# Optimization experiments

Hardware: AMD Instinct MI355X
Metric: run time of the kernel (lower is better)

The kernel has to match this reference:

```python
import jax, jax.numpy as jnp
import numpy as np
import math

L_LAYERS = 4
EMBED = 512
HEADS = 8
FFN = 2048
EPS = 1e-20
PAD_IDX = 0


def sinusoidal_table(num_embeddings, embedding_dim, padding_idx=0):
    half = embedding_dim // 2
    freq = jnp.exp(jnp.arange(half, dtype=jnp.float32) * (-math.log(10000.0) / (half - 1)))
    ang = jnp.arange(num_embeddings, dtype=jnp.float32)[:, None] * freq[None, :]
    emb = jnp.concatenate([jnp.sin(ang), jnp.cos(ang)], axis=1)
    if padding_idx is not None:
        emb = emb.at[padding_idx].set(0.0)
    return emb  # [num_embeddings, embedding_dim]


def layer_norm(x, g, b):
    mu = jnp.mean(x, axis=-1, keepdims=True)
    var = jnp.mean((x - mu) ** 2, axis=-1, keepdims=True)
    return (x - mu) * jax.lax.rsqrt(var + EPS) * g + b


def mha(x_q, x_kv, Wqkv, bqkv, Wo, bo, mask):
    """Custom attention: scaled scores, multiplicative mask, GLOBAL min-max norm (no softmax)."""
    T, B, C = x_q.shape
    S = x_kv.shape[0]
    hd = C // HEADS
    scale = hd ** -0.5
    q = x_q @ Wqkv[:C].T + bqkv[:C]
    k = x_kv @ Wqkv[C:2 * C].T + bqkv[C:2 * C]
    v = x_kv @ Wqkv[2 * C:].T + bqkv[2 * C:]
    q = q * scale
    # [T,B,C] -> [B*H, T, hd]
    q = q.reshape(T, B * HEADS, hd).transpose(1, 0, 2)
    k = k.reshape(S, B * HEADS, hd).transpose(1, 0, 2)
    v = v.reshape(S, B * HEADS, hd).transpose(1, 0, 2)
    w = jnp.einsum('bth,bsh->bts', q, k)  # [B*H, T, S]
    if mask is not None:
        w = w * mask[None, :, :]
    # global min-max normalization (as in the torch source)
    w = (w - jnp.min(w)) / (jnp.max(w) - jnp.min(w))
    a = jnp.einsum('bts,bsh->bth', w, v)  # [B*H, T, hd]
    a = a.transpose(1, 0, 2).reshape(T, B, C)
    return a @ Wo.T + bo


def setup_inputs() -> dict:
    key = jax.random.key(0)
    ks = iter(jax.random.split(key, 32))
    T, B, C, F, L = 2048, 2, EMBED, FFN, L_LAYERS
    d = {}
    d['x'] = jax.random.normal(next(ks), (T, B, C), dtype=jnp.float32)
    d['enc_out'] = jax.random.normal(next(ks), (T, B, C), dtype=jnp.float32)
    d['tokens'] = jax.random.randint(next(ks), (B, T), 0, 32000, dtype=jnp.int64 if jax.config.read('jax_enable_x64') else jnp.int32)
    sd = C ** -0.5
    d['self_Wqkv'] = jax.random.normal(next(ks), (L, 3 * C, C)) * sd
    d['self_bqkv'] = jnp.zeros((L, 3 * C))
    d['self_Wo'] = jax.random.normal(next(ks), (L, C, C)) * sd
    d['self_bo'] = jnp.zeros((L, C))
    d['cross_Wqkv'] = jax.random.normal(next(ks), (L, 3 * C, C)) * sd
    d['cross_bqkv'] = jnp.zeros((L, 3 * C))
    d['cross_Wo'] = jax.random.normal(next(ks), (L, C, C)) * sd
    d['cross_bo'] = jnp.zeros((L, C))
    d['fc1_w'] = jax.random.normal(next(ks), (L, F, C)) * sd
    d['fc1_b'] = jnp.zeros((L, F))
    d['fc2_w'] = jax.random.normal(next(ks), (L, C, F)) * (F ** -0.5)
    d['fc2_b'] = jnp.zeros((L, C))
    d['ln1_g'] = jnp.ones((L, C)); d['ln1_b'] = jnp.zeros((L, C))
    d['ln2_g'] = jnp.ones((L, C)); d['ln2_b'] = jnp.zeros((L, C))
    d['ln3_g'] = jnp.ones((L, C)); d['ln3_b'] = jnp.zeros((L, C))
    return d


def _forward(x, enc_out, tokens, self_Wqkv, self_bqkv, self_Wo, self_bo,
             cross_Wqkv, cross_bqkv, cross_Wo, cross_bo,
             fc1_w, fc1_b, fc2_w, fc2_b, ln1_g, ln1_b, ln2_g, ln2_b, ln3_g, ln3_b):
    T, B, C = x.shape
    # sinusoidal positional embedding (make_positions with padding_idx=0, no left pad)
    table = sinusoidal_table(PAD_IDX + 1 + T, C, PAD_IDX)
    pos = jnp.where(tokens != PAD_IDX, jnp.arange(1, T + 1)[None, :], 0)  # [B, T]
    pe = table[pos]  # [B, T, C]
    x = x + pe.transpose(1, 0, 2)
    # multiplicative future mask: tril of ones
    fmask = jnp.tril(jnp.ones((T, T), dtype=x.dtype))
    for l in range(L_LAYERS):
        # self-attention
        res = x
        x = mha(x, x, self_Wqkv[l], self_bqkv[l], self_Wo[l], self_bo[l], fmask)
        x = layer_norm(res + x, ln1_g[l], ln1_b[l])
        # cross-attention (no mask)
        res = x
        x = mha(x, enc_out, cross_Wqkv[l], cross_bqkv[l], cross_Wo[l], cross_bo[l], None)
        x = layer_norm(res + x, ln2_g[l], ln2_b[l])
        # FFN
        res = x
        h = jax.nn.relu(x @ fc1_w[l].T + fc1_b[l])
        x = h @ fc2_w[l].T + fc2_b[l]
        x = layer_norm(res + x, ln3_g[l], ln3_b[l])
    return x


def reference(x, enc_out, tokens, self_Wqkv, self_bqkv, self_Wo, self_bo,
              cross_Wqkv, cross_bqkv, cross_Wo, cross_bo,
              fc1_w, fc1_b, fc2_w, fc2_b, ln1_g, ln1_b, ln2_g, ln2_b, ln3_g, ln3_b):
    return _forward(x, enc_out, tokens, self_Wqkv, self_bqkv, self_Wo, self_bo,
                    cross_Wqkv, cross_bqkv, cross_Wo, cross_bo,
                    fc1_w, fc1_b, fc2_w, fc2_b, ln1_g, ln1_b, ln2_g, ln2_b, ln3_g, ln3_b)
```

## Files before the change

kernel.cpp:

```cpp
#include <hip/hip_runtime.h>
#include <math.h>

typedef __bf16 bf16;
typedef unsigned short u16;
typedef __bf16 bf16x8 __attribute__((ext_vector_type(8)));
typedef float f32x4 __attribute__((ext_vector_type(4)));

#define T_SEQ 2048
#define NB    2
#define CE    512
#define NH    8
#define HD    64
#define ROWS  4096
#define NBH   16
#define LDT   40
#define LDA   72

#define MFMA16(a,b,c) __builtin_amdgcn_mfma_f32_16x16x32_bf16((a),(b),(c),0,0,0)

static __device__ __forceinline__ int xcd_swz(int id, int n) {
  int q = n >> 3, r = n & 7;
  int x = id & 7, o = id >> 3;
  return (x < r) ? (x * (q + 1) + o) : (r * (q + 1) + (x - r) * q + o);
}

__global__ __launch_bounds__(256) void sniff(const u16* __restrict__ xs,
                                             const int* __restrict__ toks,
                                             int* __restrict__ flags)
{
  const int tid = threadIdx.x;
  int crazy = 0, ze = 0;
  for (int i = tid; i < 4096; i += 256) {
    int e = (xs[i] >> 7) & 0xFF;
    if (e >= 141) crazy++;
    if (((i & 1) == 0) && (xs[i] == 0)) ze++;
  }
  int zc = 0;
  for (int i = tid; i < 1024; i += 256)
    if (toks[2 * i + 1] == 0) zc++;
  __shared__ int r1[4], r2[4], r3[4];
#pragma unroll
  for (int o = 32; o; o >>= 1) {
    crazy += __shfl_down(crazy, o); ze += __shfl_down(ze, o); zc += __shfl_down(zc, o);
  }
  if ((tid & 63) == 0) { r1[tid >> 6] = crazy; r2[tid >> 6] = ze; r3[tid >> 6] = zc; }
  __syncthreads();
  if (tid == 0) {
    int c = r1[0] + r1[1] + r1[2] + r1[3];
    int z = r2[0] + r2[1] + r2[2] + r2[3];
    int t = r3[0] + r3[1] + r3[2] + r3[3];
    flags[0] = (z > 1500 || c > 64) ? 1 : 0;
    flags[1] = (t > 900) ? 1 : 0;
  }
}

static __device__ __forceinline__ float ldf(const void* src, size_t eoff, bool f32) {
  return f32 ? ((const float*)src)[eoff] : (float)((const bf16*)src)[eoff];
}

__global__ __launch_bounds__(256) void posembed(const void* __restrict__ xsrc,
                                                const int* __restrict__ toks,
                                                const int* __restrict__ flags,
                                                float* __restrict__ xf)
{
  const bool f32 = flags[0] != 0;
  const bool tok64 = flags[1] != 0;
  const int row = blockIdx.x;
  const int t = row >> 1, b = row & 1;
  const int tix = b * T_SEQ + t;
  const int tok = tok64 ? toks[2 * tix] : toks[tix];
  const int p = (tok != 0) ? (t + 1) : 0;
  const float kf = -0.0361193740f;
  for (int c = threadIdx.x; c < CE; c += 256) {
    float pe = 0.0f;
    if (p != 0) {
      int i = (c < 256) ? c : (c - 256);
      float freq = expf((float)i * kf);
      float ang = (float)p * freq;
      pe = (c < 256) ? sinf(ang) : cosf(ang);
    }
    xf[(size_t)row * CE + c] = ldf(xsrc, (size_t)row * CE + c, f32) + pe;
  }
}

template<bool RELUF, bool AFFINE>
__global__ __launch_bounds__(256) void gemm_mfma(const float* __restrict__ A,
                                                 const void* __restrict__ A2,
                                                 const void* __restrict__ Bw, size_t bwOff,
                                                 const void* __restrict__ bias, size_t biasOff,
                                                 const int* __restrict__ flags,
                                                 float* __restrict__ Cf,
                                                 int N, int K, int kspan,
                                                 int nbx, int nbxA,
                                                 long long partStride,
                                                 const float* __restrict__ mmf,
                                                 const float* __restrict__ vsum)
{
  __shared__ __align__(16) bf16 AhS[2][128 * LDT];
  __shared__ __align__(16) bf16 AlS[2][128 * LDT];
  __shared__ __align__(16) bf16 BhS[2][128 * LDT];
  __shared__ __align__(16) bf16 BlS[2][128 * LDT];
  const int fl = flags[0];
  const int nblk = nbx * (int)1;
  (void)nblk;
  const int id = xcd_swz((int)blockIdx.x, (int)gridDim.x);
  const int per_z = nbx * 32;
  const int zz = id / per_z;
  const int rem = id - zz * per_z;
  const int by = rem / nbx, bx = rem - by * nbx;
  const bool a_f32 = (bx < nbxA) ? true : (fl != 0);
  const void* Abase = (bx < nbxA) ? (const void*)A : A2;
  const bool b_f32 = (fl != 0);
  const int tid = threadIdx.x;
  const int m0 = by * 128, n0 = bx * 128;
  const int srow = tid >> 1;
  const int skc  = (tid & 1) * 16;
  const int wid = tid >> 6, lane = tid & 63;
  const int wm = (wid >> 1) * 64, wn = (wid & 1) * 64;
  const int fr = lane & 15;
  const int fk = (lane >> 4) * 8;
  const int kb = zz * kspan;
  const int ke = (kb + kspan < K) ? (kb + kspan) : K;
  float* Cp = Cf + (long long)zz * partStride;
  const int arow1 = (m0 + srow) & 1;
  float inv_ = 0.0f, cmn_ = 0.0f;
  if (AFFINE) { inv_ = 1.0f / (mmf[1] - mmf[0]); cmn_ = mmf[0] * inv_; }
  f32x4 acc[4][4] = {};

  uint4 ra[4], rb[4];
  auto loadA = [&](int k0) {
    size_t g = (size_t)(m0 + srow) * K + k0 + skc;
    if (a_f32) {
      const uint4* p = (const uint4*)((const float*)Abase + g);
      ra[0] = p[0]; ra[1] = p[1]; ra[2] = p[2]; ra[3] = p[3];
    } else {
      const uint4* p = (const uint4*)((const bf16*)Abase + g);
      ra[0] = p[0]; ra[1] = p[1];
    }
  };
  auto loadB = [&](int k0) {
    size_t g = bwOff + (size_t)(n0 + srow) * K + k0 + skc;
    if (b_f32) {
      const uint4* p = (const uint4*)((const float*)Bw + g);
      rb[0] = p[0]; rb[1] = p[1]; rb[2] = p[2]; rb[3] = p[3];
    } else {
      const uint4* p = (const uint4*)((const bf16*)Bw + g);
      rb[0] = p[0]; rb[1] = p[1];
    }
  };
  auto fixA = [&](int k0) {
    if (AFFINE) {
      float* f = (float*)ra;
      const float* vs = vsum + arow1 * 512 + k0 + skc;
#pragma unroll
      for (int q = 0; q < 16; q++) f[q] = inv_ * f[q] - cmn_ * vs[q];
    }
  };
  auto cvtStore = [&](const uint4* r, bool f32src, bool wantLo, bf16* Hs, bf16* Ls) {
    float v[16];
    if (f32src) {
      const float* f = (const float*)r;
#pragma unroll
      for (int q = 0; q < 16; q++) v[q] = f[q];
    } else {
      const bf16* c = (const bf16*)r;
#pragma unroll
      for (int q = 0; q < 16; q++) v[q] = (float)c[q];
    }
    bf16x8 h0, h1, l0, l1;
#pragma unroll
    for (int q = 0; q < 8; q++) {
      bf16 ha = (bf16)v[q], hb = (bf16)v[8 + q];
      h0[q] = ha; h1[q] = hb;
      l0[q] = (bf16)(v[q]     - (float)ha);
      l1[q] = (bf16)(v[8 + q] - (float)hb);
    }
    *(bf16x8*)&Hs[srow * LDT + skc]     = h0;
    *(bf16x8*)&Hs[srow * LDT + skc + 8] = h1;
    if (wantLo) {
      *(bf16x8*)&Ls[srow * LDT + skc]     = l0;
      *(bf16x8*)&Ls[srow * LDT + skc + 8] = l1;
    }
  };

  loadA(kb); loadB(kb);
  fixA(kb);
  cvtStore(ra, a_f32, a_f32, AhS[0], AlS[0]);
  cvtStore(rb, b_f32, b_f32, BhS[0], BlS[0]);
  if (kb + 32 < ke) { loadA(kb + 32); loadB(kb + 32); }

  int cur = 0;
  for (int k0 = kb; k0 < ke; k0 += 32) {
    __syncthreads();
    if (k0 + 32 < ke) {
      fixA(k0 + 32);
      cvtStore(ra, a_f32, a_f32, AhS[cur ^ 1], AlS[cur ^ 1]);
      cvtStore(rb, b_f32, b_f32, BhS[cur ^ 1], BlS[cur ^ 1]);
      if (k0 + 64 < ke) { loadA(k0 + 64); loadB(k0 + 64); }
    }
    const bf16* Ahc = AhS[cur]; const bf16* Alc = AlS[cur];
    const bf16* Bhc = BhS[cur]; const bf16* Blc = BlS[cur];
    bf16x8 ah[4], bh[4];
#pragma unroll
    for (int i = 0; i < 4; i++) ah[i] = *(const bf16x8*)&Ahc[(wm + i*16 + fr) * LDT + fk];
#pragma unroll
    for (int j = 0; j < 4; j++) bh[j] = *(const bf16x8*)&Bhc[(wn + j*16 + fr) * LDT + fk];
#pragma unroll
    for (int i = 0; i < 4; i++)
#pragma unroll
      for (int j = 0; j < 4; j++)
        acc[i][j] = MFMA16(ah[i], bh[j], acc[i][j]);
    if (a_f32) {
      bf16x8 al[4];
#pragma unroll
      for (int i = 0; i < 4; i++) al[i] = *(const bf16x8*)&Alc[(wm + i*16 + fr) * LDT + fk];
#pragma unroll
      for (int i = 0; i < 4; i++)
#pragma unroll
        for (int j = 0; j < 4; j++)
          acc[i][j] = MFMA16(al[i], bh[j], acc[i][j]);
    }
    if (b_f32) {
      bf16x8 bl[4];
#pragma unroll
      for (int j = 0; j < 4; j++) bl[j] = *(const bf16x8*)&Blc[(wn + j*16 + fr) * LDT + fk];
#pragma unroll
      for (int i = 0; i < 4; i++)
#pragma unroll
        for (int j = 0; j < 4; j++)
          acc[i][j] = MFMA16(ah[i], bl[j], acc[i][j]);
    }
    cur ^= 1;
  }
  const int orow0 = m0 + wm + (lane >> 4) * 4;
  const int ocol0 = n0 + wn + (lane & 15);
  const bool addb = (zz == 0);
#pragma unroll
  for (int j = 0; j < 4; j++) {
    int col = ocol0 + j * 16;
    float bv = addb ? ldf(bias, biasOff + col, b_f32) : 0.0f;
#pragma unroll
    for (int i = 0; i < 4; i++) {
#pragma unroll
      for (int r = 0; r < 4; r++) {
        float vv = acc[i][j][r] + bv;
        if (RELUF) vv = fmaxf(vv, 0.0f);
        Cp[(size_t)(orow0 + i * 16 + r) * N + col] = vv;
      }
    }
  }
}

__global__ __launch_bounds__(256) void prep_kv(const float* __restrict__ base, int ld,
                                               int kofs0, int vofs0,
                                               bf16* __restrict__ kh, bf16* __restrict__ kl,
                                               bf16* __restrict__ vth, bf16* __restrict__ vtl,
                                               float* __restrict__ vcs)
{
  __shared__ float ts[64 * 65];
  const int bh = blockIdx.x, s0 = blockIdx.y * 64;
  const int b = bh >> 3, h = bh & 7;
  const int kofs = kofs0 + h * HD, vofs = vofs0 + h * HD;
  const int tid = threadIdx.x;
#pragma unroll
  for (int it = 0; it < 16; ++it) {
    int idx = it * 256 + tid, r = idx >> 6, d = idx & 63;
    size_t rowb = (size_t)((s0 + r) * NB + b) * ld;
    float v = base[rowb + kofs + d];
    bf16 hi = (bf16)v;
    size_t o = ((size_t)bh * T_SEQ + s0 + r) * 64 + d;
    kh[o] = hi; kl[o] = (bf16)(v - (float)hi);
    ts[r * 65 + d] = base[rowb + vofs + d];
  }
  __syncthreads();
  const int d = tid >> 2, sseg = (tid & 3) * 16;
  bf16x8 hv0, lv0, hv1, lv1;
#pragma unroll
  for (int q = 0; q < 8; ++q) {
    float v0 = ts[(sseg + q) * 65 + d];
    float v1 = ts[(sseg + 8 + q) * 65 + d];
    bf16 h0 = (bf16)v0, h1 = (bf16)v1;
    hv0[q] = h0; lv0[q] = (bf16)(v0 - (float)h0);
    hv1[q] = h1; lv1[q] = (bf16)(v1 - (float)h1);
  }
  size_t o = ((size_t)bh * 64 + d) * T_SEQ + s0 + sseg;
  *(bf16x8*)&vth[o]     = hv0;
  *(bf16x8*)&vth[o + 8] = hv1;
  *(bf16x8*)&vtl[o]     = lv0;
  *(bf16x8*)&vtl[o + 8] = lv1;
  if (tid < 64) {
    float s = 0.0f;
    for (int j = 0; j < 64; ++j) s += ts[j * 65 + tid];
    vcs[((size_t)bh * 32 + blockIdx.y) * 64 + tid] = s;
  }
}

__device__ __forceinline__ int remap_ty(int ty) { return (ty < 16) ? ty : 47 - ty; }

template<bool MASK>
__global__ __launch_bounds__(256) void fattn(const float* __restrict__ qbase, int qld, int qofs0,
                                             const bf16* __restrict__ kh, const bf16* __restrict__ kl,
                                             const bf16* __restrict__ vth, const bf16* __restrict__ vtl,
                                             float* __restrict__ partial,
                                             float* __restrict__ pvout)
{
  __shared__ __align__(16) bf16 Qh[64 * LDA], Ql[64 * LDA];
  __shared__ __align__(16) bf16 Kh[64 * LDA], Kl[64 * LDA];
  __shared__ __align__(16) bf16 Vh[64 * LDA], Vl[64 * LDA];
  __shared__ __align__(16) bf16 Ph[64 * LDA], Pl[64 * LDA];
  __shared__ float rn[4], rx[4];
  const int id = xcd_swz((int)blockIdx.x, 512);
  const int bh = id >> 5;
  const int tyr = remap_ty(id & 31);
  const int t0 = tyr * 64;
  const int b = bh >> 3, h = bh & 7;
  const int qofs = qofs0 + h * HD;
  const int tid = threadIdx.x;
#pragma unroll
  for (int it = 0; it < 16; ++it) {
    int idx = it * 256 + tid, r = idx >> 6, d = idx & 63;
    float v = qbase[(size_t)((t0 + r) * NB + b) * qld + qofs + d] * 0.125f;
    bf16 hi = (bf16)v;
    Qh[r * LDA + d] = hi; Ql[r * LDA + d] = (bf16)(v - (float)hi);
  }
  const int wid = tid >> 6, lane = tid & 63;
  const int wm_ = (wid >> 1) * 32, wn_ = (wid & 1) * 32;
  const int fr = lane & 15, fko = (lane >> 4) * 8;
  const int crr = (lane >> 4) * 4, crc = lane & 15;
  const int cr = tid >> 2, cseg = (tid & 3) * 16;
  float mn = 1e30f, mx = -1e30f;
  f32x4 o4[2][2] = {};
  const int nch = MASK ? (tyr + 1) : 32;
  for (int sc = 0; sc < nch; ++sc) {
    const int s0 = sc * 64;
    __syncthreads();
    {
      size_t go = ((size_t)bh * T_SEQ + s0 + cr) * 64 + cseg;
      *(bf16x8*)&Kh[cr * LDA + cseg]     = *(const bf16x8*)&kh[go];
      *(bf16x8*)&Kh[cr * LDA + cseg + 8] = *(const bf16x8*)&kh[go + 8];
      *(bf16x8*)&Kl[cr * LDA + cseg]     = *(const bf16x8*)&kl[go];
      *(bf16x8*)&Kl[cr * LDA + cseg + 8] = *(const bf16x8*)&kl[go + 8];
      size_t gv = ((size_t)bh * 64 + cr) * T_SEQ + s0 + cseg;
      *(bf16x8*)&Vh[cr * LDA + cseg]     = *(const bf16x8*)&vth[gv];
      *(bf16x8*)&Vh[cr * LDA + cseg + 8] = *(const bf16x8*)&vth[gv + 8];
      *(bf16x8*)&Vl[cr * LDA + cseg]     = *(const bf16x8*)&vtl[gv];
      *(bf16x8*)&Vl[cr * LDA + cseg + 8] = *(const bf16x8*)&vtl[gv + 8];
    }
    __syncthreads();
    f32x4 a4[2][2] = {};
#pragma unroll
    for (int ks = 0; ks < 2; ++ks) {
      bf16x8 aH[2], aL[2], bH[2], bL[2];
#pragma unroll
      for (int i = 0; i < 2; ++i) {
        aH[i] = *(const bf16x8*)&Qh[(wm_ + i*16 + fr) * LDA + ks*32 + fko];
        aL[i] = *(const bf16x8*)&Ql[(wm_ + i*16 + fr) * LDA + ks*32 + fko];
        bH[i] = *(const bf16x8*)&Kh[(wn_ + i*16 + fr) * LDA + ks*32 + fko];
        bL[i] = *(const bf16x8*)&Kl[(wn_ + i*16 + fr) * LDA + ks*32 + fko];
      }
#pragma unroll
      for (int i = 0; i < 2; ++i)
#pragma unroll
        for (int j = 0; j < 2; ++j) {
          a4[i][j] = MFMA16(aH[i], bH[j], a4[i][j]);
          a4[i][j] = MFMA16(aL[i], bH[j], a4[i][j]);
          a4[i][j] = MFMA16(aH[i], bL[j], a4[i][j]);
        }
    }
#pragma unroll
    for (int i = 0; i < 2; ++i)
#pragma unroll
      for (int j = 0; j < 2; ++j)
#pragma unroll
        for (int r = 0; r < 4; ++r) {
          int tl = wm_ + i*16 + crr + r;
          int sl = wn_ + j*16 + crc;
          float w = a4[i][j][r];
          if (MASK && (s0 + sl) > (t0 + tl)) w = 0.0f;
          mn = fminf(mn, w); mx = fmaxf(mx, w);
          bf16 wh = (bf16)w;
          Ph[tl * LDA + sl] = wh;
          Pl[tl * LDA + sl] = (bf16)(w - (float)wh);
        }
    __syncthreads();
#pragma unroll
    for (int ks = 0; ks < 2; ++ks) {
      bf16x8 pH[2], pL[2], vH[2], vL[2];
#pragma unroll
      for (int i = 0; i < 2; ++i) {
        pH[i] = *(const bf16x8*)&Ph[(wm_ + i*16 + fr) * LDA + ks*32 + fko];
        pL[i] = *(const bf16x8*)&Pl[(wm_ + i*16 + fr) * LDA + ks*32 + fko];
        vH[i] = *(const bf16x8*)&Vh[(wn_ + i*16 + fr) * LDA + ks*32 + fko];
        vL[i] = *(const bf16x8*)&Vl[(wn_ + i*16 + fr) * LDA + ks*32 + fko];
      }
#pragma unroll
      for (int i = 0; i < 2; ++i)
#pragma unroll
        for (int j = 0; j < 2; ++j) {
          o4[i][j] = MFMA16(pH[i], vH[j], o4[i][j]);
          o4[i][j] = MFMA16(pL[i], vH[j], o4[i][j]);
          o4[i][j] = MFMA16(pH[i], vL[j], o4[i][j]);
        }
    }
  }
#pragma unroll
  for (int i = 0; i < 2; ++i)
#pragma unroll
    for (int j = 0; j < 2; ++j)
#pragma unroll
      for (int r = 0; r < 4; ++r) {
        int tl = wm_ + i*16 + crr + r;
        int dl = wn_ + j*16 + crc;
        pvout[(size_t)((t0 + tl) * NB + b) * CE + h * HD + dl] = o4[i][j][r];
      }
#pragma unroll
  for (int o = 32; o; o >>= 1) { mn = fminf(mn, __shfl_down(mn, o)); mx = fmaxf(mx, __shfl_down(mx, o)); }
  if (lane == 0) { rn[wid] = mn; rx[wid] = mx; }
  __syncthreads();
  if (tid == 0) {
    partial[2 * id]     = fminf(fminf(rn[0], rn[1]), fminf(rn[2], rn[3]));
    partial[2 * id + 1] = fmaxf(fmaxf(rx[0], rx[1]), fmaxf(rx[2], rx[3]));
  }
}

__global__ __launch_bounds__(512) void reduce_mm(const float* __restrict__ partial,
                                                 const float* __restrict__ vcs,
                                                 float* __restrict__ mmf,
                                                 float* __restrict__ vsum)
{
  const int tid = threadIdx.x, w = tid >> 6, l = tid & 63;
  __shared__ float rn[8], rx[8];
  float mn = partial[2 * tid], mx = partial[2 * tid + 1];
#pragma unroll
  for (int o = 32; o; o >>= 1) { mn = fminf(mn, __shfl_down(mn, o)); mx = fmaxf(mx, __shfl_down(mx, o)); }
  if (l == 0) { rn[w] = mn; rx[w] = mx; }
  __syncthreads();
  if (tid == 0) {
    float a = 1e30f, c = -1e30f;
#pragma unroll
    for (int i = 0; i < 8; i++) { a = fminf(a, rn[i]); c = fmaxf(c, rx[i]); }
    mmf[0] = a; mmf[1] = c;
  }
  for (int e = tid; e < 1024; e += 512) {
    int bh = e >> 6, d = e & 63;
    float s = 0.0f;
#pragma unroll
    for (int ch = 0; ch < 32; ++ch) s += vcs[(size_t)bh * 2048 + ch * 64 + d];
    vsum[e] = s;
  }
}

template<int NP>
__global__ __launch_bounds__(256) void ln_sum(const float* __restrict__ res,
                                              const float* __restrict__ p, long long pstride,
                                              const void* __restrict__ g, const void* __restrict__ be,
                                              size_t goff, const int* __restrict__ flags,
                                              float* __restrict__ xfo)
{
  __shared__ float red[4];
  const bool fl = flags[0] != 0;
  const int tid = threadIdx.x;
  const size_t base = (size_t)blockIdx.x * CE;
  float a  = res[base + tid];
  float b2 = res[base + tid + 256];
#pragma unroll
  for (int k = 0; k < NP; k++) {
    a  += p[(long long)k * pstride + base + tid];
    b2 += p[(long long)k * pstride + base + tid + 256];
  }
  float s = a + b2;
#pragma unroll
  for (int o = 32; o; o >>= 1) s += __shfl_down(s, o);
  if ((tid & 63) == 0) red[tid >> 6] = s;
  __syncthreads();
  float mu = (red[0] + red[1] + red[2] + red[3]) * (1.0f / 512.0f);
  __syncthreads();
  float da = a - mu, db = b2 - mu;
  float q = da * da + db * db;
#pragma unroll
  for (int o = 32; o; o >>= 1) q += __shfl_down(q, o);
  if ((tid & 63) == 0) red[tid >> 6] = q;
  __syncthreads();
  float var = (red[0] + red[1] + red[2] + red[3]) * (1.0f / 512.0f);
  float rs = rsqrtf(var + 1e-20f);
  xfo[base + tid]       = da * rs * ldf(g, goff + tid, fl)       + ldf(be, goff + tid, fl);
  xfo[base + tid + 256] = db * rs * ldf(g, goff + tid + 256, fl) + ldf(be, goff + tid + 256, fl);
}

extern "C" void kernel_launch(void* const* d_in, const int* in_sizes, int n_in,
                              void* d_out, int out_size, void* d_ws, size_t ws_size,
                              hipStream_t stream)
{
  (void)in_sizes; (void)n_in; (void)out_size; (void)ws_size;
  const void* x_in   = d_in[0];
  const void* enc_in = d_in[1];
  const int*  tokens = (const int*)d_in[2];
  const void* sWqkv = d_in[3];
  const void* sbqkv = d_in[4];
  const void* sWo   = d_in[5];
  const void* sbo   = d_in[6];
  const void* cWqkv = d_in[7];
  const void* cbqkv = d_in[8];
  const void* cWo   = d_in[9];
  const void* cbo   = d_in[10];
  const void* fc1w  = d_in[11];
  const void* fc1b  = d_in[12];
  const void* fc2w  = d_in[13];
  const void* fc2b  = d_in[14];
  const void* ln1g  = d_in[15];
  const void* ln1b  = d_in[16];
  const void* ln2g  = d_in[17];
  const void* ln2b  = d_in[18];
  const void* ln3g  = d_in[19];
  const void* ln3b  = d_in[20];

  char* ws = (char*)d_ws;
  size_t off = 0;
  auto alloc = [&](size_t bytes) -> char* {
    char* p = ws + off;
    off += (bytes + 255) & ~(size_t)255;
    return p;
  };
  int*   flags   = (int*)  alloc(256);
  float* mmf     = (float*)alloc(256);
  float* vsum    = (float*)alloc(1024 * 4);
  float* partial = (float*)alloc(4096);
  float* xf      = (float*)alloc((size_t)ROWS * CE * 4);
  float* y       = (float*)alloc((size_t)ROWS * CE * 4);
  float* qkv     = (float*)alloc((size_t)ROWS * 2048 * 4);
  float* pblk    = (float*)alloc((size_t)ROWS * CE * 4 * 4);
  bf16*  khb     = (bf16*) alloc((size_t)16 * T_SEQ * 64 * 2);
  bf16*  klb     = (bf16*) alloc((size_t)16 * T_SEQ * 64 * 2);
  bf16*  vth     = (bf16*) alloc((size_t)16 * 64 * T_SEQ * 2);
  bf16*  vtl     = (bf16*) alloc((size_t)16 * 64 * T_SEQ * 2);
  float* vcs     = (float*)alloc((size_t)16 * 32 * 64 * 4);
  const long long PS_FULL = (long long)ROWS * CE;

  sniff<<<1, 256, 0, stream>>>((const u16*)x_in, tokens, flags);
  posembed<<<ROWS, 256, 0, stream>>>(x_in, tokens, flags, xf);

  for (int l = 0; l < 4; l++) {
    gemm_mfma<false, false><<<384, 256, 0, stream>>>(
        xf, xf, sWqkv, (size_t)l * 1536 * 512, sbqkv, (size_t)l * 1536, flags, qkv,
        1536, 512, 512, 12, 12, 0, nullptr, nullptr);
    prep_kv<<<dim3(16, 32), 256, 0, stream>>>(qkv, 1536, 512, 1024, khb, klb, vth, vtl, vcs);
    fattn<true><<<512, 256, 0, stream>>>(qkv, 1536, 0, khb, klb, vth, vtl, partial, y);
    reduce_mm<<<1, 512, 0, stream>>>(partial, vcs, mmf, vsum);
    gemm_mfma<false, true><<<512, 256, 0, stream>>>(
        y, y, sWo, (size_t)l * 512 * 512, sbo, (size_t)l * 512, flags, pblk,
        512, 512, 128, 4, 4, PS_FULL, mmf, vsum);
    ln_sum<4><<<ROWS, 256, 0, stream>>>(xf, pblk, PS_FULL, ln1g, ln1b, (size_t)l * 512, flags, xf);

    gemm_mfma<false, false><<<384, 256, 0, stream>>>(
        xf, enc_in, cWqkv, (size_t)l * 1536 * 512, cbqkv, (size_t)l * 1536, flags, qkv,
        1536, 512, 512, 12, 4 , 0, nullptr, nullptr);
    prep_kv<<<dim3(16, 32), 256, 0, stream>>>(qkv, 1536, 512, 1024, khb, klb, vth, vtl, vcs);
    fattn<false><<<512, 256, 0, stream>>>(qkv, 1536, 0, khb, klb, vth, vtl, partial, y);
    reduce_mm<<<1, 512, 0, stream>>>(partial, vcs, mmf, vsum);
    gemm_mfma<false, true><<<512, 256, 0, stream>>>(
        y, y, cWo, (size_t)l * 512 * 512, cbo, (size_t)l * 512, flags, pblk,
        512, 512, 128, 4, 4, PS_FULL, mmf, vsum);
    ln_sum<4><<<ROWS, 256, 0, stream>>>(xf, pblk, PS_FULL, ln2g, ln2b, (size_t)l * 512, flags, xf);

    gemm_mfma<true, false><<<512, 256, 0, stream>>>(
        xf, xf, fc1w, (size_t)l * 2048 * 512, fc1b, (size_t)l * 2048, flags, qkv,
        2048, 512, 512, 16, 16, 0, nullptr, nullptr);
    gemm_mfma<false, false><<<512, 256, 0, stream>>>(
        qkv, qkv, fc2w, (size_t)l * 512 * 2048, fc2b, (size_t)l * 512, flags, pblk,
        512, 2048, 512, 4, 4, PS_FULL, nullptr, nullptr);
    float* lnout = (l == 3) ? (float*)d_out : xf;
    ln_sum<4><<<ROWS, 256, 0, stream>>>(xf, pblk, PS_FULL, ln3g, ln3b, (size_t)l * 512, flags, lnout);
  }
}
```

Baseline: 2.602 ms.

## Pre-split activations and weights into bf16 hi/lo pairs, move min-max affine to epilogue

Producers (posembed, ln_sum, fattn, fc1 epilogue) now write bf16 hi/lo pairs, and a one-time wprep kernel splits all weights and enc_out into hi/lo buffers. The GEMM becomes a pure bf16 loader with no fp32 loads or conversion in its main loop, and it skips the lo MFMA passes when the flags show the lo parts are zero. The min-max affine on attention output moves out of the Wo GEMM into a small wo_term kernel plus ln_sum. This trades extra memory writes and the per-call weight preparation against lighter GEMM inner loops.

```diff
diff --git a/kernel.cpp b/kernel.cpp
--- a/kernel.cpp
+++ b/kernel.cpp
@@ -9,19 +9,29 @@
 #define T_SEQ 2048
 #define NB    2
 #define CE    512
-#define NH    8
 #define HD    64
 #define ROWS  4096
-#define NBH   16
 #define LDT   40
 #define LDA   72
 
 #define MFMA16(a,b,c) __builtin_amdgcn_mfma_f32_16x16x32_bf16((a),(b),(c),0,0,0)
+
+#define O_SQ  0LL
+#define O_SWO 3145728LL
+#define O_CQ  4194304LL
+#define O_CWO 7340032LL
+#define O_F1  8388608LL
+#define O_F2  12582912LL
+#define O_E   16777216LL
 
 static __device__ __forceinline__ int xcd_swz(int id, int n) {
   int q = n >> 3, r = n & 7;
   int x = id & 7, o = id >> 3;
   return (x < r) ? (x * (q + 1) + o) : (r * (q + 1) + (x - r) * q + o);
+}
+
+static __device__ __forceinline__ float ldf(const void* src, size_t eoff, bool f32) {
+  return f32 ? ((const float*)src)[eoff] : (float)((const bf16*)src)[eoff];
 }
 
 __global__ __launch_bounds__(256) void sniff(const u16* __restrict__ xs,
@@ -51,17 +61,65 @@
     int t = r3[0] + r3[1] + r3[2] + r3[3];
     flags[0] = (z > 1500 || c > 64) ? 1 : 0;
     flags[1] = (t > 900) ? 1 : 0;
-  }
-}
-
-static __device__ __forceinline__ float ldf(const void* src, size_t eoff, bool f32) {
-  return f32 ? ((const float*)src)[eoff] : (float)((const bf16*)src)[eoff];
+    flags[2] = 1;
+    flags[3] = 0;
+    flags[4] = 0;
+  }
+}
+
+__global__ __launch_bounds__(256) void wprep(const void* w0, const void* w1, const void* w2,
+                                             const void* w3, const void* w4, const void* w5,
+                                             const void* w6,
+                                             bf16* __restrict__ wh, bf16* __restrict__ wl,
+                                             int* __restrict__ flags)
+{
+  const int m = blockIdx.y;
+  const void* srcs[7] = {w0, w1, w2, w3, w4, w5, w6};
+  const int sizes[7]  = {3145728, 1048576, 3145728, 1048576, 4194304, 4194304, 2097152};
+  const long long offs[7] = {O_SQ, O_SWO, O_CQ, O_CWO, O_F1, O_F2, O_E};
+  const void* src = srcs[m];
+  const int sz = sizes[m];
+  const long long off = offs[m];
+  const bool fl = flags[0] != 0;
+  long long i0 = ((long long)blockIdx.x * 256 + threadIdx.x) * 16;
+  bool nz = false;
+  if (i0 < sz) {
+    float v[16];
+    if (fl) {
+      const float4* p = (const float4*)((const float*)src + i0);
+#pragma unroll
+      for (int q = 0; q < 4; q++) { float4 t = p[q]; v[4*q] = t.x; v[4*q+1] = t.y; v[4*q+2] = t.z; v[4*q+3] = t.w; }
+    } else {
+      const uint4* p = (const uint4*)((const bf16*)src + i0);
+      uint4 a = p[0], b = p[1];
+      const bf16* c0 = (const bf16*)&a; const bf16* c1 = (const bf16*)&b;
+#pragma unroll
+      for (int q = 0; q < 8; q++) { v[q] = (float)c0[q]; v[8+q] = (float)c1[q]; }
+    }
+    bf16x8 h0, h1, l0, l1;
+#pragma unroll
+    for (int q = 0; q < 8; q++) {
+      bf16 a = (bf16)v[q], b = (bf16)v[8+q];
+      h0[q] = a; h1[q] = b;
+      float la = v[q] - (float)a, lb = v[8+q] - (float)b;
+      l0[q] = (bf16)la; l1[q] = (bf16)lb;
+      nz = nz || (la != 0.0f) || (lb != 0.0f);
+    }
+    *(bf16x8*)&wh[off + i0]     = h0;
+    *(bf16x8*)&wh[off + i0 + 8] = h1;
+    *(bf16x8*)&wl[off + i0]     = l0;
+    *(bf16x8*)&wl[off + i0 + 8] = l1;
+  }
+  unsigned long long mv = __ballot(nz);
+  if ((threadIdx.x & 63) == 0 && mv)
+    atomicOr(&flags[(m == 6) ? 3 : 4], 1);
 }
 
 __global__ __launch_bounds__(256) void posembed(const void* __restrict__ xsrc,
                                                 const int* __restrict__ toks,
                                                 const int* __restrict__ flags,
-                                                float* __restrict__ xf)
+                                                float* __restrict__ xf,
+                                                bf16* __restrict__ xh, bf16* __restrict__ xl)
 {
   const bool f32 = flags[0] != 0;
   const bool tok64 = flags[1] != 0;
@@ -79,124 +137,87 @@
       float ang = (float)p * freq;
       pe = (c < 256) ? sinf(ang) : cosf(ang);
     }
-    xf[(size_t)row * CE + c] = ldf(xsrc, (size_t)row * CE + c, f32) + pe;
-  }
-}
-
-template<bool RELUF, bool AFFINE>
-__global__ __launch_bounds__(256) void gemm_mfma(const float* __restrict__ A,
-                                                 const void* __restrict__ A2,
-                                                 const void* __restrict__ Bw, size_t bwOff,
-                                                 const void* __restrict__ bias, size_t biasOff,
-                                                 const int* __restrict__ flags,
-                                                 float* __restrict__ Cf,
-                                                 int N, int K, int kspan,
-                                                 int nbx, int nbxA,
-                                                 long long partStride,
-                                                 const float* __restrict__ mmf,
-                                                 const float* __restrict__ vsum)
+    float v = ldf(xsrc, (size_t)row * CE + c, f32) + pe;
+    size_t o = (size_t)row * CE + c;
+    xf[o] = v;
+    bf16 hi = (bf16)v;
+    xh[o] = hi; xl[o] = (bf16)(v - (float)hi);
+  }
+}
+
+template<int OUTM, bool BIAS>
+__global__ __launch_bounds__(256) void gemm_bb(const bf16* __restrict__ A1h, const bf16* __restrict__ A1l,
+                                               const bf16* __restrict__ A2h, const bf16* __restrict__ A2l,
+                                               const bf16* __restrict__ Bhg, const bf16* __restrict__ Blg,
+                                               long long bOff,
+                                               const void* __restrict__ bias, size_t biasOff,
+                                               const int* __restrict__ flags,
+                                               int aIdx1, int aIdx2, int bIdx,
+                                               float* __restrict__ Cf,
+                                               bf16* __restrict__ Coh, bf16* __restrict__ Col,
+                                               int N, int K, int kspan, int nbx, int nbxA,
+                                               long long partStride)
 {
   __shared__ __align__(16) bf16 AhS[2][128 * LDT];
   __shared__ __align__(16) bf16 AlS[2][128 * LDT];
   __shared__ __align__(16) bf16 BhS[2][128 * LDT];
   __shared__ __align__(16) bf16 BlS[2][128 * LDT];
-  const int fl = flags[0];
-  const int nblk = nbx * (int)1;
-  (void)nblk;
   const int id = xcd_swz((int)blockIdx.x, (int)gridDim.x);
   const int per_z = nbx * 32;
   const int zz = id / per_z;
   const int rem = id - zz * per_z;
   const int by = rem / nbx, bx = rem - by * nbx;
-  const bool a_f32 = (bx < nbxA) ? true : (fl != 0);
-  const void* Abase = (bx < nbxA) ? (const void*)A : A2;
-  const bool b_f32 = (fl != 0);
+  const bf16* Ahg = (bx < nbxA) ? A1h : A2h;
+  const bf16* Alg = (bx < nbxA) ? A1l : A2l;
+  const bool alo = flags[(bx < nbxA) ? aIdx1 : aIdx2] != 0;
+  const bool blo = flags[bIdx] != 0;
+  const bool bfl = flags[0] != 0;
   const int tid = threadIdx.x;
   const int m0 = by * 128, n0 = bx * 128;
-  const int srow = tid >> 1;
-  const int skc  = (tid & 1) * 16;
+  const int srow = tid >> 1, skc = (tid & 1) * 16;
   const int wid = tid >> 6, lane = tid & 63;
   const int wm = (wid >> 1) * 64, wn = (wid & 1) * 64;
-  const int fr = lane & 15;
-  const int fk = (lane >> 4) * 8;
+  const int fr = lane & 15, fk = (lane >> 4) * 8;
   const int kb = zz * kspan;
   const int ke = (kb + kspan < K) ? (kb + kspan) : K;
-  float* Cp = Cf + (long long)zz * partStride;
-  const int arow1 = (m0 + srow) & 1;
-  float inv_ = 0.0f, cmn_ = 0.0f;
-  if (AFFINE) { inv_ = 1.0f / (mmf[1] - mmf[0]); cmn_ = mmf[0] * inv_; }
   f32x4 acc[4][4] = {};
 
-  uint4 ra[4], rb[4];
-  auto loadA = [&](int k0) {
-    size_t g = (size_t)(m0 + srow) * K + k0 + skc;
-    if (a_f32) {
-      const uint4* p = (const uint4*)((const float*)Abase + g);
-      ra[0] = p[0]; ra[1] = p[1]; ra[2] = p[2]; ra[3] = p[3];
-    } else {
-      const uint4* p = (const uint4*)((const bf16*)Abase + g);
-      ra[0] = p[0]; ra[1] = p[1];
-    }
+  uint4 rah[2], ral[2], rbh[2], rbl[2];
+  auto loadAB = [&](int k0) {
+    size_t ga = (size_t)(m0 + srow) * K + k0 + skc;
+    const uint4* pa = (const uint4*)(Ahg + ga);
+    rah[0] = pa[0]; rah[1] = pa[1];
+    if (alo) { const uint4* q = (const uint4*)(Alg + ga); ral[0] = q[0]; ral[1] = q[1]; }
+    size_t gb = (size_t)bOff + (size_t)(n0 + srow) * K + k0 + skc;
+    const uint4* pb = (const uint4*)(Bhg + gb);
+    rbh[0] = pb[0]; rbh[1] = pb[1];
+    if (blo) { const uint4* q = (const uint4*)(Blg + gb); rbl[0] = q[0]; rbl[1] = q[1]; }
   };
-  auto loadB = [&](int k0) {
-    size_t g = bwOff + (size_t)(n0 + srow) * K + k0 + skc;
-    if (b_f32) {
-      const uint4* p = (const uint4*)((const float*)Bw + g);
-      rb[0] = p[0]; rb[1] = p[1]; rb[2] = p[2]; rb[3] = p[3];
-    } else {
-      const uint4* p = (const uint4*)((const bf16*)Bw + g);
-      rb[0] = p[0]; rb[1] = p[1];
+  auto storeAB = [&](int buf) {
+    *(uint4*)&AhS[buf][srow * LDT + skc]     = rah[0];
+    *(uint4*)&AhS[buf][srow * LDT + skc + 8] = rah[1];
+    if (alo) {
+      *(uint4*)&AlS[buf][srow * LDT + skc]     = ral[0];
+      *(uint4*)&AlS[buf][srow * LDT + skc + 8] = ral[1];
+    }
+    *(uint4*)&BhS[buf][srow * LDT + skc]     = rbh[0];
+    *(uint4*)&BhS[buf][srow * LDT + skc + 8] = rbh[1];
+    if (blo) {
+      *(uint4*)&BlS[buf][srow * LDT + skc]     = rbl[0];
+      *(uint4*)&BlS[buf][srow * LDT + skc + 8] = rbl[1];
     }
   };
-  auto fixA = [&](int k0) {
-    if (AFFINE) {
-      float* f = (float*)ra;
-      const float* vs = vsum + arow1 * 512 + k0 + skc;
-#pragma unroll
-      for (int q = 0; q < 16; q++) f[q] = inv_ * f[q] - cmn_ * vs[q];
-    }
-  };
-  auto cvtStore = [&](const uint4* r, bool f32src, bool wantLo, bf16* Hs, bf16* Ls) {
-    float v[16];
-    if (f32src) {
-      const float* f = (const float*)r;
-#pragma unroll
-      for (int q = 0; q < 16; q++) v[q] = f[q];
-    } else {
-      const bf16* c = (const bf16*)r;
-#pragma unroll
-      for (int q = 0; q < 16; q++) v[q] = (float)c[q];
-    }
-    bf16x8 h0, h1, l0, l1;
-#pragma unroll
-    for (int q = 0; q < 8; q++) {
-      bf16 ha = (bf16)v[q], hb = (bf16)v[8 + q];
-      h0[q] = ha; h1[q] = hb;
-      l0[q] = (bf16)(v[q]     - (float)ha);
-      l1[q] = (bf16)(v[8 + q] - (float)hb);
-    }
-    *(bf16x8*)&Hs[srow * LDT + skc]     = h0;
-    *(bf16x8*)&Hs[srow * LDT + skc + 8] = h1;
-    if (wantLo) {
-      *(bf16x8*)&Ls[srow * LDT + skc]     = l0;
-      *(bf16x8*)&Ls[srow * LDT + skc + 8] = l1;
-    }
-  };
-
-  loadA(kb); loadB(kb);
-  fixA(kb);
-  cvtStore(ra, a_f32, a_f32, AhS[0], AlS[0]);
-  cvtStore(rb, b_f32, b_f32, BhS[0], BlS[0]);
-  if (kb + 32 < ke) { loadA(kb + 32); loadB(kb + 32); }
+
+  loadAB(kb);
+  storeAB(0);
+  if (kb + 32 < ke) loadAB(kb + 32);
 
   int cur = 0;
   for (int k0 = kb; k0 < ke; k0 += 32) {
     __syncthreads();
     if (k0 + 32 < ke) {
-      fixA(k0 + 32);
-      cvtStore(ra, a_f32, a_f32, AhS[cur ^ 1], AlS[cur ^ 1]);
-      cvtStore(rb, b_f32, b_f32, BhS[cur ^ 1], BlS[cur ^ 1]);
-      if (k0 + 64 < ke) { loadA(k0 + 64); loadB(k0 + 64); }
+      storeAB(cur ^ 1);
+      if (k0 + 64 < ke) loadAB(k0 + 64);
     }
     const bf16* Ahc = AhS[cur]; const bf16* Alc = AlS[cur];
     const bf16* Bhc = BhS[cur]; const bf16* Blc = BlS[cur];
@@ -210,7 +231,7 @@
 #pragma unroll
       for (int j = 0; j < 4; j++)
         acc[i][j] = MFMA16(ah[i], bh[j], acc[i][j]);
-    if (a_f32) {
+    if (alo) {
       bf16x8 al[4];
 #pragma unroll
       for (int i = 0; i < 4; i++) al[i] = *(const bf16x8*)&Alc[(wm + i*16 + fr) * LDT + fk];
@@ -220,7 +241,7 @@
         for (int j = 0; j < 4; j++)
           acc[i][j] = MFMA16(al[i], bh[j], acc[i][j]);
     }
-    if (b_f32) {
+    if (blo) {
       bf16x8 bl[4];
 #pragma unroll
       for (int j = 0; j < 4; j++) bl[j] = *(const bf16x8*)&Blc[(wn + j*16 + fr) * LDT + fk];
@@ -234,19 +255,33 @@
   }
   const int orow0 = m0 + wm + (lane >> 4) * 4;
   const int ocol0 = n0 + wn + (lane & 15);
-  const bool addb = (zz == 0);
-#pragma unroll
-  for (int j = 0; j < 4; j++) {
-    int col = ocol0 + j * 16;
-    float bv = addb ? ldf(bias, biasOff + col, b_f32) : 0.0f;
-#pragma unroll
-    for (int i = 0; i < 4; i++) {
-#pragma unroll
-      for (int r = 0; r < 4; r++) {
-        float vv = acc[i][j][r] + bv;
-        if (RELUF) vv = fmaxf(vv, 0.0f);
-        Cp[(size_t)(orow0 + i * 16 + r) * N + col] = vv;
-      }
+  if (OUTM == 0) {
+    float* Cp = Cf + (long long)zz * partStride;
+    const bool addb = BIAS && (zz == 0);
+#pragma unroll
+    for (int j = 0; j < 4; j++) {
+      int col = ocol0 + j * 16;
+      float bv = addb ? ldf(bias, biasOff + col, bfl) : 0.0f;
+#pragma unroll
+      for (int i = 0; i < 4; i++)
+#pragma unroll
+        for (int r = 0; r < 4; r++)
+          Cp[(size_t)(orow0 + i * 16 + r) * N + col] = acc[i][j][r] + bv;
+    }
+  } else {
+#pragma unroll
+    for (int j = 0; j < 4; j++) {
+      int col = ocol0 + j * 16;
+      float bv = ldf(bias, biasOff + col, bfl);
+#pragma unroll
+      for (int i = 0; i < 4; i++)
+#pragma unroll
+        for (int r = 0; r < 4; r++) {
+          float vv = fmaxf(acc[i][j][r] + bv, 0.0f);
+          bf16 hi = (bf16)vv;
+          size_t o = (size_t)(orow0 + i * 16 + r) * N + col;
+          Coh[o] = hi; Col[o] = (bf16)(vv - (float)hi);
+        }
     }
   }
 }
@@ -259,8 +294,8 @@
 {
   __shared__ float ts[64 * 65];
   const int bh = blockIdx.x, s0 = blockIdx.y * 64;
-  const int b = bh >> 3, h = bh & 7;
-  const int kofs = kofs0 + h * HD, vofs = vofs0 + h * HD;
+  const int b = bh >> 3, hq = bh & 7;
+  const int kofs = kofs0 + hq * HD, vofs = vofs0 + hq * HD;
   const int tid = threadIdx.x;
 #pragma unroll
   for (int it = 0; it < 16; ++it) {
@@ -302,7 +337,7 @@
                                              const bf16* __restrict__ kh, const bf16* __restrict__ kl,
                                              const bf16* __restrict__ vth, const bf16* __restrict__ vtl,
                                              float* __restrict__ partial,
-                                             float* __restrict__ pvout)
+                                             bf16* __restrict__ pvh, bf16* __restrict__ pvl)
 {
   __shared__ __align__(16) bf16 Qh[64 * LDA], Ql[64 * LDA];
   __shared__ __align__(16) bf16 Kh[64 * LDA], Kl[64 * LDA];
@@ -313,8 +348,8 @@
   const int bh = id >> 5;
   const int tyr = remap_ty(id & 31);
   const int t0 = tyr * 64;
-  const int b = bh >> 3, h = bh & 7;
-  const int qofs = qofs0 + h * HD;
+  const int b = bh >> 3, hq = bh & 7;
+  const int qofs = qofs0 + hq * HD;
   const int tid = threadIdx.x;
 #pragma unroll
   for (int it = 0; it < 16; ++it) {
@@ -411,7 +446,10 @@
       for (int r = 0; r < 4; ++r) {
         int tl = wm_ + i*16 + crr + r;
         int dl = wn_ + j*16 + crc;
-        pvout[(size_t)((t0 + tl) * NB + b) * CE + h * HD + dl] = o4[i][j][r];
+        float val = o4[i][j][r];
+        bf16 hi = (bf16)val;
+        size_t o = (size_t)((t0 + tl) * NB + b) * CE + hq * HD + dl;
+        pvh[o] = hi; pvl[o] = (bf16)(val - (float)hi);
       }
 #pragma unroll
   for (int o = 32; o; o >>= 1) { mn = fminf(mn, __shfl_down(mn, o)); mx = fmaxf(mx, __shfl_down(mx, o)); }
@@ -450,23 +488,53 @@
   }
 }
 
-template<int NP>
+__global__ __launch_bounds__(256) void wo_term(const float* __restrict__ mmf,
+                                               const float* __restrict__ vsum,
+                                               const void* __restrict__ Wo, size_t woOff,
+                                               const void* __restrict__ bo, size_t boOff,
+                                               const int* __restrict__ flags,
+                                               float* __restrict__ term)
+{
+  const bool fl = flags[0] != 0;
+  const float inv = 1.0f / (mmf[1] - mmf[0]);
+  const float cmn = mmf[0] * inv;
+  int idx = blockIdx.x * 256 + threadIdx.x;
+  int b = idx >> 9, c = idx & 511;
+  float s = 0.0f;
+  for (int k = 0; k < 512; k++)
+    s += vsum[b * 512 + k] * ldf(Wo, woOff + (size_t)c * 512 + k, fl);
+  term[idx] = -cmn * s + ldf(bo, boOff + c, fl);
+}
+
+template<int NP, bool AFF, bool SPLIT>
 __global__ __launch_bounds__(256) void ln_sum(const float* __restrict__ res,
                                               const float* __restrict__ p, long long pstride,
                                               const void* __restrict__ g, const void* __restrict__ be,
                                               size_t goff, const int* __restrict__ flags,
-                                              float* __restrict__ xfo)
+                                              const float* __restrict__ mmf,
+                                              const float* __restrict__ term,
+                                              float* __restrict__ xfo,
+                                              bf16* __restrict__ xh, bf16* __restrict__ xl)
 {
   __shared__ float red[4];
   const bool fl = flags[0] != 0;
   const int tid = threadIdx.x;
   const size_t base = (size_t)blockIdx.x * CE;
-  float a  = res[base + tid];
-  float b2 = res[base + tid + 256];
+  float pa = 0.0f, pb = 0.0f;
 #pragma unroll
   for (int k = 0; k < NP; k++) {
-    a  += p[(long long)k * pstride + base + tid];
-    b2 += p[(long long)k * pstride + base + tid + 256];
+    pa += p[(long long)k * pstride + base + tid];
+    pb += p[(long long)k * pstride + base + tid + 256];
+  }
+  float a, b2;
+  if (AFF) {
+    const float inv = 1.0f / (mmf[1] - mmf[0]);
+    const int b = blockIdx.x & 1;
+    a  = res[base + tid]       + inv * pa + term[b * 512 + tid];
+    b2 = res[base + tid + 256] + inv * pb + term[b * 512 + tid + 256];
+  } else {
+    a  = res[base + tid]       + pa;
+    b2 = res[base + tid + 256] + pb;
   }
   float s = a + b2;
 #pragma unroll
@@ -483,8 +551,15 @@
   __syncthreads();
   float var = (red[0] + red[1] + red[2] + red[3]) * (1.0f / 512.0f);
   float rs = rsqrtf(var + 1e-20f);
-  xfo[base + tid]       = da * rs * ldf(g, goff + tid, fl)       + ldf(be, goff + tid, fl);
-  xfo[base + tid + 256] = db * rs * ldf(g, goff + tid + 256, fl) + ldf(be, goff + tid + 256, fl);
+  float o1 = da * rs * ldf(g, goff + tid, fl)       + ldf(be, goff + tid, fl);
+  float o2 = db * rs * ldf(g, goff + tid + 256, fl) + ldf(be, goff + tid + 256, fl);
+  xfo[base + tid]       = o1;
+  xfo[base + tid + 256] = o2;
+  if (SPLIT) {
+    bf16 h1 = (bf16)o1, h2 = (bf16)o2;
+    xh[base + tid]       = h1; xl[base + tid]       = (bf16)(o1 - (float)h1);
+    xh[base + tid + 256] = h2; xl[base + tid + 256] = (bf16)(o2 - (float)h2);
+  }
 }
 
 extern "C" void kernel_launch(void* const* d_in, const int* in_sizes, int n_in,
@@ -525,50 +600,79 @@
   float* mmf     = (float*)alloc(256);
   float* vsum    = (float*)alloc(1024 * 4);
   float* partial = (float*)alloc(4096);
+  float* term    = (float*)alloc(1024 * 4);
   float* xf      = (float*)alloc((size_t)ROWS * CE * 4);
-  float* y       = (float*)alloc((size_t)ROWS * CE * 4);
+  bf16*  xh      = (bf16*) alloc((size_t)ROWS * CE * 2);
+  bf16*  xl      = (bf16*) alloc((size_t)ROWS * CE * 2);
   float* qkv     = (float*)alloc((size_t)ROWS * 2048 * 4);
+  bf16*  pvh     = (bf16*) alloc((size_t)ROWS * CE * 2);
+  bf16*  pvl     = (bf16*) alloc((size_t)ROWS * CE * 2);
   float* pblk    = (float*)alloc((size_t)ROWS * CE * 4 * 4);
   bf16*  khb     = (bf16*) alloc((size_t)16 * T_SEQ * 64 * 2);
   bf16*  klb     = (bf16*) alloc((size_t)16 * T_SEQ * 64 * 2);
   bf16*  vth     = (bf16*) alloc((size_t)16 * 64 * T_SEQ * 2);
   bf16*  vtl     = (bf16*) alloc((size_t)16 * 64 * T_SEQ * 2);
   float* vcs     = (float*)alloc((size_t)16 * 32 * 64 * 4);
+  bf16*  wh      = (bf16*) alloc((size_t)18874368 * 2);
+  bf16*  wl      = (bf16*) alloc((size_t)18874368 * 2);
+  bf16* hh = (bf16*)qkv;
+  bf16* hl = (bf16*)qkv + (size_t)ROWS * 2048;
   const long long PS_FULL = (long long)ROWS * CE;
 
   sniff<<<1, 256, 0, stream>>>((const u16*)x_in, tokens, flags);
-  posembed<<<ROWS, 256, 0, stream>>>(x_in, tokens, flags, xf);
+  posembed<<<ROWS, 256, 0, stream>>>(x_in, tokens, flags, xf, xh, xl);
+  wprep<<<dim3(1024, 7), 256, 0, stream>>>(sWqkv, sWo, cWqkv, cWo, fc1w, fc2w, enc_in,
+                                           wh, wl, flags);
 
   for (int l = 0; l < 4; l++) {
-    gemm_mfma<false, false><<<384, 256, 0, stream>>>(
-        xf, xf, sWqkv, (size_t)l * 1536 * 512, sbqkv, (size_t)l * 1536, flags, qkv,
-        1536, 512, 512, 12, 12, 0, nullptr, nullptr);
+    gemm_bb<0, true><<<384, 256, 0, stream>>>(
+        xh, xl, xh, xl, wh, wl, O_SQ + (long long)l * 786432,
+        sbqkv, (size_t)l * 1536, flags, 2, 2, 4,
+        qkv, nullptr, nullptr, 1536, 512, 512, 12, 12, 0);
     prep_kv<<<dim3(16, 32), 256, 0, stream>>>(qkv, 1536, 512, 1024, khb, klb, vth, vtl, vcs);
-    fattn<true><<<512, 256, 0, stream>>>(qkv, 1536, 0, khb, klb, vth, vtl, partial, y);
+    fattn<true><<<512, 256, 0, stream>>>(qkv, 1536, 0, khb, klb, vth, vtl, partial, pvh, pvl);
     reduce_mm<<<1, 512, 0, stream>>>(partial, vcs, mmf, vsum);
-    gemm_mfma<false, true><<<512, 256, 0, stream>>>(
-        y, y, sWo, (size_t)l * 512 * 512, sbo, (size_t)l * 512, flags, pblk,
-        512, 512, 128, 4, 4, PS_FULL, mmf, vsum);
-    ln_sum<4><<<ROWS, 256, 0, stream>>>(xf, pblk, PS_FULL, ln1g, ln1b, (size_t)l * 512, flags, xf);
-
-    gemm_mfma<false, false><<<384, 256, 0, stream>>>(
-        xf, enc_in, cWqkv, (size_t)l * 1536 * 512, cbqkv, (size_t)l * 1536, flags, qkv,
-        1536, 512, 512, 12, 4 , 0, nullptr, nullptr);
+    wo_term<<<4, 256, 0, stream>>>(mmf, vsum, sWo, (size_t)l * 262144, sbo, (size_t)l * 512,
+                                   flags, term);
+    gemm_bb<0, false><<<512, 256, 0, stream>>>(
+        pvh, pvl, pvh, pvl, wh, wl, O_SWO + (long long)l * 262144,
+        sbo, 0, flags, 2, 2, 4,
+        pblk, nullptr, nullptr, 512, 512, 128, 4, 4, PS_FULL);
+    ln_sum<4, true, true><<<ROWS, 256, 0, stream>>>(
+        xf, pblk, PS_FULL, ln1g, ln1b, (size_t)l * 512, flags, mmf, term, xf, xh, xl);
+
+    gemm_bb<0, true><<<384, 256, 0, stream>>>(
+        xh, xl, wh + O_E, wl + O_E, wh, wl, O_CQ + (long long)l * 786432,
+        cbqkv, (size_t)l * 1536, flags, 2, 3, 4,
+        qkv, nullptr, nullptr, 1536, 512, 512, 12, 4, 0);
     prep_kv<<<dim3(16, 32), 256, 0, stream>>>(qkv, 1536, 512, 1024, khb, klb, vth, vtl, vcs);
-    fattn<false><<<512, 256, 0, stream>>>(qkv, 1536, 0, khb, klb, vth, vtl, partial, y);
+    fattn<false><<<512, 256, 0, stream>>>(qkv, 1536, 0, khb, klb, vth, vtl, partial, pvh, pvl);
     reduce_mm<<<1, 512, 0, stream>>>(partial, vcs, mmf, vsum);
-    gemm_mfma<false, true><<<512, 256, 0, stream>>>(
-        y, y, cWo, (size_t)l * 512 * 512, cbo, (size_t)l * 512, flags, pblk,
-        512, 512, 128, 4, 4, PS_FULL, mmf, vsum);
-    ln_sum<4><<<ROWS, 256, 0, stream>>>(xf, pblk, PS_FULL, ln2g, ln2b, (size_t)l * 512, flags, xf);
-
-    gemm_mfma<true, false><<<512, 256, 0, stream>>>(
-        xf, xf, fc1w, (size_t)l * 2048 * 512, fc1b, (size_t)l * 2048, flags, qkv,
-        2048, 512, 512, 16, 16, 0, nullptr, nullptr);
-    gemm_mfma<false, false><<<512, 256, 0, stream>>>(
-        qkv, qkv, fc2w, (size_t)l * 512 * 2048, fc2b, (size_t)l * 512, flags, pblk,
-        512, 2048, 512, 4, 4, PS_FULL, nullptr, nullptr);
-    float* lnout = (l == 3) ? (float*)d_out : xf;
-    ln_sum<4><<<ROWS, 256, 0, stream>>>(xf, pblk, PS_FULL, ln3g, ln3b, (size_t)l * 512, flags, lnout);
-  }
-}
+    wo_term<<<4, 256, 0, stream>>>(mmf, vsum, cWo, (size_t)l * 262144, cbo, (size_t)l * 512,
+                                   flags, term);
+    gemm_bb<0, false><<<512, 256, 0, stream>>>(
+        pvh, pvl, pvh, pvl, wh, wl, O_CWO + (long long)l * 262144,
+        cbo, 0, flags, 2, 2, 4,
+        pblk, nullptr, nullptr, 512, 512, 128, 4, 4, PS_FULL);
+    ln_sum<4, true, true><<<ROWS, 256, 0, stream>>>(
+        xf, pblk, PS_FULL, ln2g, ln2b, (size_t)l * 512, flags, mmf, term, xf, xh, xl);
+
+    gemm_bb<1, true><<<512, 256, 0, stream>>>(
+        xh, xl, xh, xl, wh, wl, O_F1 + (long long)l * 1048576,
+        fc1b, (size_t)l * 2048, flags, 2, 2, 4,
+        nullptr, hh, hl, 2048, 512, 512, 16, 16, 0);
+    gemm_bb<0, true><<<512, 256, 0, stream>>>(
+        hh, hl, hh, hl, wh, wl, O_F2 + (long long)l * 1048576,
+        fc2b, (size_t)l * 512, flags, 2, 2, 4,
+        pblk, nullptr, nullptr, 512, 2048, 512, 4, 4, PS_FULL);
+    if (l == 3) {
+      ln_sum<4, false, false><<<ROWS, 256, 0, stream>>>(
+          xf, pblk, PS_FULL, ln3g, ln3b, (size_t)l * 512, flags, nullptr, nullptr,
+          (float*)d_out, nullptr, nullptr);
+    } else {
+      ln_sum<4, false, true><<<ROWS, 256, 0, stream>>>(
+          xf, pblk, PS_FULL, ln3g, ln3b, (size_t)l * 512, flags, nullptr, nullptr,
+          xf, xh, xl);
+    }
+  }
+}
```

New measurement: 3.214 ms. +23.5%, slower.
